# Optimization experiments

Hardware: AMD Instinct MI355X
Metric: run time of the kernel (lower is better)

## Reference

```python
import jax, jax.numpy as jnp
import numpy as np

N = 8192
F_IN = 128
F_OUT = 64
E = 262144
NEG_SLOPE = 0.01  # torch LeakyReLU default
MASK_VAL = -1e9


def setup_inputs() -> dict:
    key = jax.random.key(0)
    k1, k2, k3, k4 = jax.random.split(key, 4)
    x = jax.random.normal(k1, (N, F_IN), dtype=jnp.float32)
    edge_index = jax.random.randint(k2, (2, E), 0, N, dtype=jnp.int64)
    # xavier-uniform-like init for params
    W = jax.random.normal(k3, (F_IN, F_OUT), dtype=jnp.float32) * (1.0 / np.sqrt(F_IN))
    a = jax.random.normal(k4, (2 * F_OUT, 1), dtype=jnp.float32) * (1.0 / np.sqrt(2 * F_OUT))
    b = jnp.zeros((F_OUT,), dtype=jnp.float32)
    return {"x": x, "edge_index": edge_index, "W": W, "a": a, "b": b}


def reference(x, edge_index, W, a, b):
    n = x.shape[0]
    wh = x @ W  # [N, F_OUT]
    # e[i, j] = wh_i . a_src + wh_j . a_dst  (column + row broadcast -> N x N)
    e_src = wh @ a[:F_OUT]          # [N, 1]
    e_dst = (wh @ a[F_OUT:]).T       # [1, N]
    e = jax.nn.leaky_relu(e_src + e_dst, NEG_SLOPE)  # [N, N]
    # dense adjacency from edge list (to_dense_adj) + self loops
    adj = jnp.zeros((n, n), dtype=x.dtype).at[edge_index[0], edge_index[1]].add(1.0)
    adj = adj + jnp.eye(n, dtype=x.dtype)
    attention = jax.nn.softmax(jnp.where(adj > 0, e, MASK_VAL), axis=1)
    out = attention @ wh + b  # bias.flatten() broadcast over rows
    return out
```

## Files before the change

### kernel.cpp

```cpp
#include <hip/hip_runtime.h>
#include <math.h>


#define F_IN  128
#define F_OUT 64

__global__ void zero_kernel(uint4* __restrict__ p, int nvec) {
    int t = blockIdx.x * blockDim.x + threadIdx.x;
    if (t < nvec) p[t] = make_uint4(0u, 0u, 0u, 0u);
}

__global__ __launch_bounds__(256) void wh_kernel(
        const float* __restrict__ x, const float* __restrict__ W,
        const float* __restrict__ a, float* __restrict__ wh,
        float* __restrict__ s_src, float* __restrict__ s_dst) {
    __shared__ float xs[4][F_IN];
    const int wave = threadIdx.x >> 6;
    const int lane = threadIdx.x & 63;
    const int row  = blockIdx.x * 4 + wave;

    xs[wave][lane]      = x[row * F_IN + lane];
    xs[wave][lane + 64] = x[row * F_IN + 64 + lane];
    __syncthreads();

    float acc = 0.f;
    #pragma unroll
    for (int k = 0; k < F_IN; ++k)
        acc = fmaf(xs[wave][k], W[k * F_OUT + lane], acc);

    wh[row * F_OUT + lane] = acc;

    float v0 = acc * a[lane];
    float v1 = acc * a[64 + lane];
    #pragma unroll
    for (int off = 32; off; off >>= 1) {
        v0 += __shfl_down(v0, off, 64);
        v1 += __shfl_down(v1, off, 64);
    }
    if (lane == 0) { s_src[row] = v0; s_dst[row] = v1; }
}

__global__ void adj_kernel(const int* __restrict__ ei,
                           unsigned* __restrict__ bitmap, int n, int e) {
    int t = blockIdx.x * blockDim.x + threadIdx.x;
    if (t < e) {
        int i = ei[t];
        int j = ei[e + t];
        atomicOr(&bitmap[(size_t)i * 256 + (j >> 5)], 1u << (j & 31));
    } else if (t < e + n) {
        int i = t - e;
        atomicOr(&bitmap[(size_t)i * 256 + (i >> 5)], 1u << (i & 31));
    }
}

__global__ __launch_bounds__(256) void gat_row_kernel(
        const float* __restrict__ wh, const float* __restrict__ s_src,
        const float* __restrict__ s_dst, const unsigned* __restrict__ bitmap,
        const float* __restrict__ bias, float* __restrict__ out) {
    __shared__ int   lj[4][256];
    __shared__ float lzs[4][256];
    __shared__ int   lcnt[4];

    const int wave = threadIdx.x >> 6;
    const int lane = threadIdx.x & 63;
    const int row  = blockIdx.x * 4 + wave;

    if (lane == 0) lcnt[wave] = 0;
    __syncthreads();

    const float si = s_src[row];
    const uint4 wv = *(const uint4*)(bitmap + (size_t)row * 256 + lane * 4);
    unsigned wsv[4] = { wv.x, wv.y, wv.z, wv.w };

    float zmax = -INFINITY;
    #pragma unroll
    for (int w = 0; w < 4; ++w) {
        unsigned word = wsv[w];
        while (word) {
            int bpos = __ffs(word) - 1;
            word &= word - 1;
            int j = lane * 128 + w * 32 + bpos;
            float z = si + s_dst[j];
            zmax = fmaxf(zmax, z);
            int pos = atomicAdd(&lcnt[wave], 1);
            if (pos < 256) { lj[wave][pos] = j; lzs[wave][pos] = z; }
        }
    }

    #pragma unroll
    for (int off = 32; off; off >>= 1)
        zmax = fmaxf(zmax, __shfl_xor(zmax, off, 64));

    __syncthreads();

    int cnt = lcnt[wave];
    if (cnt > 256) cnt = 256;
    const float m = zmax > 0.f ? zmax : 0.01f * zmax;

    float denom = 0.f, acc = 0.f;
    for (int d = 0; d < cnt; ++d) {
        int   j = lj[wave][d];
        float z = lzs[wave][d];
        float lr = z > 0.f ? z : 0.01f * z;
        float wgt = __expf(lr - m);
        denom += wgt;
        acc = fmaf(wgt, wh[j * F_OUT + lane], acc);
    }

    out[row * F_OUT + lane] = acc / denom + bias[lane];
}

extern "C" void kernel_launch(void* const* d_in, const int* in_sizes, int n_in,
                              void* d_out, int out_size, void* d_ws, size_t ws_size,
                              hipStream_t stream) {
    const float* x  = (const float*)d_in[0];
    const int*   ei = (const int*)d_in[1];
    const float* W  = (const float*)d_in[2];
    const float* a  = (const float*)d_in[3];
    const float* b  = (const float*)d_in[4];
    float* out = (float*)d_out;

    const int n = in_sizes[0] / F_IN;
    const int e = in_sizes[1] / 2;

    char* ws = (char*)d_ws;
    float*    wh     = (float*)ws;
    float*    s_src  = (float*)(ws + (size_t)n * F_OUT * 4);
    float*    s_dst  = s_src + n;
    unsigned* bitmap = (unsigned*)((char*)(s_dst + n));

    int nvec = n * 256 / 4;
    zero_kernel<<<(nvec + 255) / 256, 256, 0, stream>>>((uint4*)bitmap, nvec);

    wh_kernel<<<n / 4, 256, 0, stream>>>(x, W, a, wh, s_src, s_dst);

    int tot = e + n;
    adj_kernel<<<(tot + 255) / 256, 256, 0, stream>>>(ei, bitmap, n, e);

    gat_row_kernel<<<n / 4, 256, 0, stream>>>(wh, s_src, s_dst, bitmap, b, out);
}
```

Measured before the change: 98.98 us.

## Fuse bitmap zeroing into wh kernel, block rows, scan-compact neighbors, parallelize softmax

The bitmap zeroing moves into the projection kernel, removing one launch. The projection now computes 16 rows per block with float4 shared loads, so each W load is reused across four rows. In the row kernel, a wave-wide prefix scan of popcounts replaces the shared atomic counter and both __syncthreads calls. The exp weights are computed in parallel across lanes and stored before an unrolled-by-4 gather loop. This cuts serialized exp work and atomic contention but adds scan overhead and extra shared-memory writes.

```diff
diff --git a/kernel.cpp b/kernel.cpp
--- a/kernel.cpp
+++ b/kernel.cpp
@@ -5,39 +5,66 @@
 #define F_IN  128
 #define F_OUT 64
 
-__global__ void zero_kernel(uint4* __restrict__ p, int nvec) {
-    int t = blockIdx.x * blockDim.x + threadIdx.x;
-    if (t < nvec) p[t] = make_uint4(0u, 0u, 0u, 0u);
-}
-
 __global__ __launch_bounds__(256) void wh_kernel(
         const float* __restrict__ x, const float* __restrict__ W,
         const float* __restrict__ a, float* __restrict__ wh,
-        float* __restrict__ s_src, float* __restrict__ s_dst) {
-    __shared__ float xs[4][F_IN];
-    const int wave = threadIdx.x >> 6;
-    const int lane = threadIdx.x & 63;
-    const int row  = blockIdx.x * 4 + wave;
+        float* __restrict__ s_src, float* __restrict__ s_dst,
+        uint4* __restrict__ bm_zero) {
+    __shared__ float xs[16][F_IN];
+    const int wave  = threadIdx.x >> 6;
+    const int lane  = threadIdx.x & 63;
+    const int rbase = blockIdx.x * 16;
 
-    xs[wave][lane]      = x[row * F_IN + lane];
-    xs[wave][lane + 64] = x[row * F_IN + 64 + lane];
+    {
+        uint4* p = bm_zero + (size_t)blockIdx.x * 1024;
+        #pragma unroll
+        for (int i = 0; i < 4; ++i)
+            p[threadIdx.x + i * 256] = make_uint4(0u, 0u, 0u, 0u);
+    }
+
+    {
+        const float4* xg = (const float4*)(x + (size_t)rbase * F_IN);
+        float4* xl = (float4*)&xs[0][0];
+        xl[threadIdx.x]       = xg[threadIdx.x];
+        xl[threadIdx.x + 256] = xg[threadIdx.x + 256];
+    }
     __syncthreads();
 
-    float acc = 0.f;
+    const int r0 = wave * 4;
+    float acc0 = 0.f, acc1 = 0.f, acc2 = 0.f, acc3 = 0.f;
+
+    #pragma unroll 8
+    for (int k4 = 0; k4 < 32; ++k4) {
+        const float4 xa = *(const float4*)&xs[r0 + 0][k4 * 4];
+        const float4 xb = *(const float4*)&xs[r0 + 1][k4 * 4];
+        const float4 xc = *(const float4*)&xs[r0 + 2][k4 * 4];
+        const float4 xd = *(const float4*)&xs[r0 + 3][k4 * 4];
+        const float w0 = W[(k4 * 4 + 0) * F_OUT + lane];
+        const float w1 = W[(k4 * 4 + 1) * F_OUT + lane];
+        const float w2 = W[(k4 * 4 + 2) * F_OUT + lane];
+        const float w3 = W[(k4 * 4 + 3) * F_OUT + lane];
+        acc0 = fmaf(xa.x, w0, fmaf(xa.y, w1, fmaf(xa.z, w2, fmaf(xa.w, w3, acc0))));
+        acc1 = fmaf(xb.x, w0, fmaf(xb.y, w1, fmaf(xb.z, w2, fmaf(xb.w, w3, acc1))));
+        acc2 = fmaf(xc.x, w0, fmaf(xc.y, w1, fmaf(xc.z, w2, fmaf(xc.w, w3, acc2))));
+        acc3 = fmaf(xd.x, w0, fmaf(xd.y, w1, fmaf(xd.z, w2, fmaf(xd.w, w3, acc3))));
+    }
+
+    const float a0 = a[lane];
+    const float a1 = a[64 + lane];
+    float accs[4] = {acc0, acc1, acc2, acc3};
     #pragma unroll
-    for (int k = 0; k < F_IN; ++k)
-        acc = fmaf(xs[wave][k], W[k * F_OUT + lane], acc);
-
-    wh[row * F_OUT + lane] = acc;
-
-    float v0 = acc * a[lane];
-    float v1 = acc * a[64 + lane];
-    #pragma unroll
-    for (int off = 32; off; off >>= 1) {
-        v0 += __shfl_down(v0, off, 64);
-        v1 += __shfl_down(v1, off, 64);
+    for (int r = 0; r < 4; ++r) {
+        const int row = rbase + r0 + r;
+        wh[(size_t)row * F_OUT + lane] = accs[r];
+        float v0 = accs[r] * a0;
+        float v1 = accs[r] * a1;
+        #pragma unroll
+        for (int off = 32; off; off >>= 1) {
+            v0 += __shfl_down(v0, off, 64);
+            v1 += __shfl_down(v1, off, 64);
+        }
+        if (lane == 0) { s_src[row] = v0; s_dst[row] = v1; }
     }
-    if (lane == 0) { s_src[row] = v0; s_dst[row] = v1; }
 }
 
 __global__ void adj_kernel(const int* __restrict__ ei,
@@ -58,56 +85,80 @@
         const float* __restrict__ s_dst, const unsigned* __restrict__ bitmap,
         const float* __restrict__ bias, float* __restrict__ out) {
     __shared__ int   lj[4][256];
-    __shared__ float lzs[4][256];
-    __shared__ int   lcnt[4];
+    __shared__ float lw[4][256];
 
     const int wave = threadIdx.x >> 6;
     const int lane = threadIdx.x & 63;
     const int row  = blockIdx.x * 4 + wave;
 
-    if (lane == 0) lcnt[wave] = 0;
-    __syncthreads();
+    const float si = s_src[row];
+    const float bv = bias[lane];
+    const uint4 wv = *(const uint4*)(bitmap + (size_t)row * 256 + lane * 4);
+    unsigned ws4[4] = { wv.x, wv.y, wv.z, wv.w };
 
-    const float si = s_src[row];
-    const uint4 wv = *(const uint4*)(bitmap + (size_t)row * 256 + lane * 4);
-    unsigned wsv[4] = { wv.x, wv.y, wv.z, wv.w };
+    int cnt_lane = __popc(wv.x) + __popc(wv.y) + __popc(wv.z) + __popc(wv.w);
+    int scan = cnt_lane;
+    #pragma unroll
+    for (int off = 1; off < 64; off <<= 1) {
+        int t = __shfl_up(scan, off, 64);
+        if (lane >= off) scan += t;
+    }
+    int total = __shfl(scan, 63, 64);
+    int pos = scan - cnt_lane;
 
     float zmax = -INFINITY;
     #pragma unroll
     for (int w = 0; w < 4; ++w) {
-        unsigned word = wsv[w];
+        unsigned word = ws4[w];
         while (word) {
-            int bpos = __ffs(word) - 1;
+            int b = __ffs(word) - 1;
             word &= word - 1;
-            int j = lane * 128 + w * 32 + bpos;
+            int j = lane * 128 + w * 32 + b;
             float z = si + s_dst[j];
             zmax = fmaxf(zmax, z);
-            int pos = atomicAdd(&lcnt[wave], 1);
-            if (pos < 256) { lj[wave][pos] = j; lzs[wave][pos] = z; }
+            if (pos < 256) { lj[wave][pos] = j; lw[wave][pos] = z; }
+            pos++;
         }
     }
+    if (total > 256) total = 256;
 
     #pragma unroll
     for (int off = 32; off; off >>= 1)
         zmax = fmaxf(zmax, __shfl_xor(zmax, off, 64));
-
-    __syncthreads();
-
-    int cnt = lcnt[wave];
-    if (cnt > 256) cnt = 256;
     const float m = zmax > 0.f ? zmax : 0.01f * zmax;
 
-    float denom = 0.f, acc = 0.f;
-    for (int d = 0; d < cnt; ++d) {
-        int   j = lj[wave][d];
-        float z = lzs[wave][d];
+    float dpart = 0.f;
+    for (int d = lane; d < total; d += 64) {
+        float z  = lw[wave][d];
         float lr = z > 0.f ? z : 0.01f * z;
-        float wgt = __expf(lr - m);
-        denom += wgt;
-        acc = fmaf(wgt, wh[j * F_OUT + lane], acc);
+        float wg = __expf(lr - m);
+        lw[wave][d] = wg;
+        dpart += wg;
     }
+    #pragma unroll
+    for (int off = 32; off; off >>= 1)
+        dpart += __shfl_xor(dpart, off, 64);
 
-    out[row * F_OUT + lane] = acc / denom + bias[lane];
+    float acc = 0.f;
+    int d = 0;
+    for (; d + 4 <= total; d += 4) {
+        int   j0 = lj[wave][d],     j1 = lj[wave][d + 1];
+        int   j2 = lj[wave][d + 2], j3 = lj[wave][d + 3];
+        float w0 = lw[wave][d],     w1 = lw[wave][d + 1];
+        float w2 = lw[wave][d + 2], w3 = lw[wave][d + 3];
+        float g0 = wh[(size_t)j0 * F_OUT + lane];
+        float g1 = wh[(size_t)j1 * F_OUT + lane];
+        float g2 = wh[(size_t)j2 * F_OUT + lane];
+        float g3 = wh[(size_t)j3 * F_OUT + lane];
+        acc = fmaf(w0, g0, acc);
+        acc = fmaf(w1, g1, acc);
+        acc = fmaf(w2, g2, acc);
+        acc = fmaf(w3, g3, acc);
+    }
+    for (; d < total; ++d)
+        acc = fmaf(lw[wave][d], wh[(size_t)lj[wave][d] * F_OUT + lane], acc);
+
+    out[(size_t)row * F_OUT + lane] = acc / dpart + bv;
 }
 
 extern "C" void kernel_launch(void* const* d_in, const int* in_sizes, int n_in,
@@ -129,10 +180,7 @@
     float*    s_dst  = s_src + n;
     unsigned* bitmap = (unsigned*)((char*)(s_dst + n));
 
-    int nvec = n * 256 / 4;
-    zero_kernel<<<(nvec + 255) / 256, 256, 0, stream>>>((uint4*)bitmap, nvec);
-
-    wh_kernel<<<n / 4, 256, 0, stream>>>(x, W, a, wh, s_src, s_dst);
+    wh_kernel<<<n / 16, 256, 0, stream>>>(x, W, a, wh, s_src, s_dst, (uint4*)bitmap);
 
     int tot = e + n;
     adj_kernel<<<(tot + 255) / 256, 256, 0, stream>>>(ei, bitmap, n, e);
```

Result: no change. 97.78 us (-1.2%).
